# Optimization experiments

Hardware: AMD Instinct MI355X
Metric: run time of the kernel (lower is better)

The kernel has to match this reference:

```python
import jax, jax.numpy as jnp
import numpy as np

GROUP_SIZE = 128


def _unpack_int4(packed):
    # packed: [..., P] int32, each holding 8 int4 nibbles (LSB-first).
    u = jax.lax.bitcast_convert_type(packed, jnp.uint32)
    shifts = jnp.arange(8, dtype=jnp.uint32) * 4  # nibble bit offsets
    vals = (u[..., None] >> shifts) & jnp.uint32(15)  # [..., P, 8]
    return vals.reshape(*packed.shape[:-1], -1)  # [..., P*8] in [0, 15]


def setup_inputs() -> dict:
    key = jax.random.key(0)
    k1, k2, k3, k4 = jax.random.split(key, 4)
    B, S, K, O = 4, 16, 4096, 11008
    G = K // GROUP_SIZE          # 32 groups
    GP = (G + 7) // 8            # 4 packed-zero columns
    imax = np.iinfo(np.int32).max
    x = jax.random.normal(k1, (B, S, K), dtype=jnp.float16)
    qweight_i32 = jax.random.randint(k2, (O, K // 8), 0, imax, dtype=jnp.int32)
    qzeros_i32 = jax.random.randint(k3, (O, GP), 0, imax, dtype=jnp.int32)
    scales_f16 = jax.random.uniform(k4, (O, G), dtype=jnp.float16,
                                    minval=0.001, maxval=0.02)
    return {"x": x, "qweight_i32": qweight_i32, "qzeros_i32": qzeros_i32,
            "scales_f16": scales_f16}


def reference(x, qweight_i32, qzeros_i32, scales_f16):
    O, G = scales_f16.shape
    K = G * GROUP_SIZE
    # Dequantize: w = (q - z) * s, per-group int4 quantization.
    q = _unpack_int4(qweight_i32)[:, :K].astype(jnp.float16)       # [O, K]
    z = _unpack_int4(qzeros_i32)[:, :G].astype(jnp.float16)        # [O, G]
    z_k = jnp.repeat(z, GROUP_SIZE, axis=1)                        # [O, K]
    s_k = jnp.repeat(scales_f16, GROUP_SIZE, axis=1)               # [O, K]
    w = (q - z_k) * s_k                                            # fp16 [O, K]
    x2d = x.reshape(-1, K).astype(jnp.float16)                     # [m, K]
    out = jnp.matmul(x2d, w.T).astype(jnp.float32)                 # [m, O]
    return out.reshape(*x.shape[:-1], O)
```

## Files before the change

kernel.cpp:

```cpp
#include <hip/hip_runtime.h>
#include <stdint.h>

typedef _Float16 half8  __attribute__((ext_vector_type(8)));
typedef _Float16 half2v __attribute__((ext_vector_type(2)));
typedef float    floatx4 __attribute__((ext_vector_type(4)));
typedef uint32_t uint4v  __attribute__((ext_vector_type(4)));

#define KDIM   4096
#define ODIM   11008
#define NG     32
#define K8     512
#define KU     (KDIM/8)
#define KSPLIT 8
#define GPB    4
#define OBLK   172

__global__ void zero_out_kernel(float4* __restrict__ out) {
    out[(size_t)blockIdx.x * 256 + threadIdx.x] = float4{0.f, 0.f, 0.f, 0.f};
}

__device__ __forceinline__ uint32_t pk_f16(float a, float b) {
    return __builtin_bit_cast(uint32_t, __builtin_amdgcn_cvt_pkrtz(a, b));
}

__global__ __launch_bounds__(256) void cvt_x_kernel(
    const float4* __restrict__ x, uint4v* __restrict__ xh)
{
    const size_t i = (size_t)blockIdx.x * 256 + threadIdx.x;
    const float4 f0 = x[2 * i];
    const float4 f1 = x[2 * i + 1];
    xh[i] = uint4v{pk_f16(f0.x, f0.y), pk_f16(f0.z, f0.w),
                   pk_f16(f1.x, f1.y), pk_f16(f1.z, f1.w)};
}

struct GBuf { uint4v a[4]; uint4v u[4]; };

__global__ __launch_bounds__(256, 4) void w4a16_kernel(
    const uint4v*   __restrict__ xh,
    const uint32_t* __restrict__ qw,
    const uint32_t* __restrict__ qz,
    const float*    __restrict__ sc,
    float*          __restrict__ out)
{
    const int t    = threadIdx.x;
    const int wv   = t >> 6;
    const int lane = t & 63;
    const int q    = lane >> 4;
    const int ml   = lane & 15;

    const int ob = blockIdx.x % OBLK;
    const int kb = blockIdx.x / OBLK;
    const int o0 = ob * 64;
    const int g0 = kb * GPB;
    const int m  = wv * 16 + ml;

    const uint4v*   xp  = xh + (size_t)m * KU + (size_t)g0 * 16 + q * 4;
    const uint32_t* qwp = qw + (size_t)(o0 + ml) * K8 + (size_t)g0 * 16 + q * 4;

    uint32_t zdw[4];
    floatx4  svec[4];
    #pragma unroll
    for (int sub = 0; sub < 4; ++sub) {
        const int o = o0 + sub * 16 + ml;
        zdw[sub]  = qz[(size_t)o * 4 + (g0 >> 3)];
        svec[sub] = *reinterpret_cast<const floatx4*>(sc + (size_t)o * NG + g0);
    }
    const int zsh0 = (kb & 1) * 16;

    floatx4 acc[4] = {{0.f,0.f,0.f,0.f},{0.f,0.f,0.f,0.f},
                      {0.f,0.f,0.f,0.f},{0.f,0.f,0.f,0.f}};

    GBuf buf[2];

    auto load_g = [&](int g, GBuf& B) {
        #pragma unroll
        for (int ks = 0; ks < 4; ++ks)
            B.a[ks] = xp[g * 16 + ks];
        #pragma unroll
        for (int sub = 0; sub < 4; ++sub)
            B.u[sub] = *reinterpret_cast<const uint4v*>(
                qwp + (size_t)sub * 16 * K8 + g * 16);
    };

    load_g(0, buf[0]);

    #pragma unroll
    for (int g = 0; g < GPB; ++g) {
        if (g + 1 < GPB) load_g(g + 1, buf[(g + 1) & 1]);
        GBuf& B = buf[g & 1];

        half8 afrag[4];
        #pragma unroll
        for (int ks = 0; ks < 4; ++ks)
            afrag[ks] = __builtin_bit_cast(half8, B.a[ks]);

        #pragma unroll
        for (int sub = 0; sub < 4; ++sub) {
            const uint32_t zh = 0x6400u | ((zdw[sub] >> (zsh0 + g * 4)) & 0xFu);
            const half2v   cz = __builtin_bit_cast(half2v, zh | (zh << 16));
            const float    s  = svec[sub][g];

            floatx4 tmp = {0.f, 0.f, 0.f, 0.f};
            #pragma unroll
            for (int ks = 0; ks < 4; ++ks) {
                const uint32_t ud = B.u[sub][ks];
                const uint32_t t0 = ( ud        & 0x000F000Fu) | 0x64006400u;
                const uint32_t t1 = ((ud >> 4)  & 0x000F000Fu) | 0x64006400u;
                const uint32_t t2 = ((ud >> 8)  & 0x000F000Fu) | 0x64006400u;
                const uint32_t t3 = ((ud >> 12) & 0x000F000Fu) | 0x64006400u;
                const uint32_t p0 = __builtin_amdgcn_perm(t1, t0, 0x05040100u);
                const uint32_t p1 = __builtin_amdgcn_perm(t3, t2, 0x05040100u);
                const uint32_t p2 = __builtin_amdgcn_perm(t1, t0, 0x07060302u);
                const uint32_t p3 = __builtin_amdgcn_perm(t3, t2, 0x07060302u);
                const half2v w0 = __builtin_bit_cast(half2v, p0) - cz;
                const half2v w1 = __builtin_bit_cast(half2v, p1) - cz;
                const half2v w2 = __builtin_bit_cast(half2v, p2) - cz;
                const half2v w3 = __builtin_bit_cast(half2v, p3) - cz;
                const uint4v bw = {__builtin_bit_cast(uint32_t, w0),
                                   __builtin_bit_cast(uint32_t, w1),
                                   __builtin_bit_cast(uint32_t, w2),
                                   __builtin_bit_cast(uint32_t, w3)};
                const half8 b = __builtin_bit_cast(half8, bw);
                tmp = __builtin_amdgcn_mfma_f32_16x16x32_f16(afrag[ks], b, tmp, 0, 0, 0);
            }
            acc[sub][0] += s * tmp[0];
            acc[sub][1] += s * tmp[1];
            acc[sub][2] += s * tmp[2];
            acc[sub][3] += s * tmp[3];
        }
    }

    const int mrow = wv * 16 + q * 4;
    #pragma unroll
    for (int sub = 0; sub < 4; ++sub) {
        float* op = out + (size_t)mrow * ODIM + (o0 + sub * 16 + ml);
        atomicAdd(op,                  acc[sub][0]);
        atomicAdd(op + (size_t)ODIM,   acc[sub][1]);
        atomicAdd(op + 2*(size_t)ODIM, acc[sub][2]);
        atomicAdd(op + 3*(size_t)ODIM, acc[sub][3]);
    }
}

extern "C" void kernel_launch(void* const* d_in, const int* in_sizes, int n_in,
                              void* d_out, int out_size, void* d_ws, size_t ws_size,
                              hipStream_t stream) {
    const float*    x       = (const float*)d_in[0];
    const uint32_t* qweight = (const uint32_t*)d_in[1];
    const uint32_t* qzeros  = (const uint32_t*)d_in[2];
    const float*    scales  = (const float*)d_in[3];
    float* out = (float*)d_out;
    uint4v* xh = (uint4v*)d_ws;

    cvt_x_kernel<<<dim3(128), dim3(256), 0, stream>>>((const float4*)x, xh);
    zero_out_kernel<<<dim3(688), dim3(256), 0, stream>>>((float4*)out);
    w4a16_kernel<<<dim3(OBLK * KSPLIT), dim3(256), 0, stream>>>(
        xh, qweight, qzeros, scales, out);
}
```

Baseline: 110.1 us.

## Fold zero-point subtraction into precomputed activation group sums

The int4 dequant now feeds the raw 1024+q fp16 values straight into the MFMA. The 1024+zero offset is removed afterwards using per-group activation sums that the conversion kernel computes and stores transposed. The x fp16 layout is interleaved so each nibble lines up with its activation without perm instructions. The K split doubles, with fewer groups per block. This trades the per-element subtract and permute work for an extra sum buffer, more atomics, and possible precision loss from the large 1024 offset in fp16/fp32 cancellation.

Result: slower. 122.7 us (+11.5%).

```diff
diff --git a/kernel.cpp b/kernel.cpp
--- a/kernel.cpp
+++ b/kernel.cpp
@@ -2,7 +2,7 @@
 #include <stdint.h>
 
 typedef _Float16 half8  __attribute__((ext_vector_type(8)));
-typedef _Float16 half2v __attribute__((ext_vector_type(2)));
+typedef float    floatx2 __attribute__((ext_vector_type(2)));
 typedef float    floatx4 __attribute__((ext_vector_type(4)));
 typedef uint32_t uint4v  __attribute__((ext_vector_type(4)));
 
@@ -10,9 +10,9 @@
 #define ODIM   11008
 #define NG     32
 #define K8     512
-#define KU     (KDIM/8)
-#define KSPLIT 8
-#define GPB    4
+#define KU     512
+#define KSPLIT 16
+#define GPB    2
 #define OBLK   172
 
 __global__ void zero_out_kernel(float4* __restrict__ out) {
@@ -24,13 +24,26 @@
 }
 
 __global__ __launch_bounds__(256) void cvt_x_kernel(
-    const float4* __restrict__ x, uint4v* __restrict__ xh)
+    const float4* __restrict__ x, uint4v* __restrict__ xh,
+    float* __restrict__ xsumT)
 {
     const size_t i = (size_t)blockIdx.x * 256 + threadIdx.x;
     const float4 f0 = x[2 * i];
     const float4 f1 = x[2 * i + 1];
-    xh[i] = uint4v{pk_f16(f0.x, f0.y), pk_f16(f0.z, f0.w),
-                   pk_f16(f1.x, f1.y), pk_f16(f1.z, f1.w)};
+    xh[i] = uint4v{pk_f16(f0.x, f1.x), pk_f16(f0.y, f1.y),
+                   pk_f16(f0.z, f1.z), pk_f16(f0.w, f1.w)};
+
+    float p = f0.x + f0.y + f0.z + f0.w + f1.x + f1.y + f1.z + f1.w;
+    p += __shfl_xor(p, 1);
+    p += __shfl_xor(p, 2);
+    p += __shfl_xor(p, 4);
+    p += __shfl_xor(p, 8);
+    if ((threadIdx.x & 15) == 0) {
+        const size_t k0 = i * 8;
+        const int m = (int)(k0 >> 12);
+        const int g = (int)(k0 >> 7) & 31;
+        xsumT[g * 64 + m] = p;
+    }
 }
 
 struct GBuf { uint4v a[4]; uint4v u[4]; };
@@ -40,6 +53,7 @@
     const uint32_t* __restrict__ qw,
     const uint32_t* __restrict__ qz,
     const float*    __restrict__ sc,
+    const float*    __restrict__ xsumT,
     float*          __restrict__ out)
 {
     const int t    = threadIdx.x;
@@ -58,20 +72,25 @@
     const uint32_t* qwp = qw + (size_t)(o0 + ml) * K8 + (size_t)g0 * 16 + q * 4;
 
     uint32_t zdw[4];
-    floatx4  svec[4];
+    floatx2  svec[4];
     #pragma unroll
     for (int sub = 0; sub < 4; ++sub) {
         const int o = o0 + sub * 16 + ml;
         zdw[sub]  = qz[(size_t)o * 4 + (g0 >> 3)];
-        svec[sub] = *reinterpret_cast<const floatx4*>(sc + (size_t)o * NG + g0);
+        svec[sub] = *reinterpret_cast<const floatx2*>(sc + (size_t)o * NG + g0);
     }
-    const int zsh0 = (kb & 1) * 16;
+    const int zsh0 = (g0 & 7) * 4;
+
+    const int mrow = wv * 16 + q * 4;
+    floatx4 xsv[GPB];
+    #pragma unroll
+    for (int g = 0; g < GPB; ++g)
+        xsv[g] = *reinterpret_cast<const floatx4*>(xsumT + (g0 + g) * 64 + mrow);
 
     floatx4 acc[4] = {{0.f,0.f,0.f,0.f},{0.f,0.f,0.f,0.f},
                       {0.f,0.f,0.f,0.f},{0.f,0.f,0.f,0.f}};
 
     GBuf buf[2];
-
     auto load_g = [&](int g, GBuf& B) {
         #pragma unroll
         for (int ks = 0; ks < 4; ++ks)
@@ -96,41 +115,30 @@
 
         #pragma unroll
         for (int sub = 0; sub < 4; ++sub) {
-            const uint32_t zh = 0x6400u | ((zdw[sub] >> (zsh0 + g * 4)) & 0xFu);
-            const half2v   cz = __builtin_bit_cast(half2v, zh | (zh << 16));
+            const uint32_t zn = (zdw[sub] >> (zsh0 + g * 4)) & 0xFu;
             const float    s  = svec[sub][g];
+            const float    czs = s * (1024.0f + (float)zn);
 
             floatx4 tmp = {0.f, 0.f, 0.f, 0.f};
             #pragma unroll
             for (int ks = 0; ks < 4; ++ks) {
                 const uint32_t ud = B.u[sub][ks];
-                const uint32_t t0 = ( ud        & 0x000F000Fu) | 0x64006400u;
-                const uint32_t t1 = ((ud >> 4)  & 0x000F000Fu) | 0x64006400u;
-                const uint32_t t2 = ((ud >> 8)  & 0x000F000Fu) | 0x64006400u;
-                const uint32_t t3 = ((ud >> 12) & 0x000F000Fu) | 0x64006400u;
-                const uint32_t p0 = __builtin_amdgcn_perm(t1, t0, 0x05040100u);
-                const uint32_t p1 = __builtin_amdgcn_perm(t3, t2, 0x05040100u);
-                const uint32_t p2 = __builtin_amdgcn_perm(t1, t0, 0x07060302u);
-                const uint32_t p3 = __builtin_amdgcn_perm(t3, t2, 0x07060302u);
-                const half2v w0 = __builtin_bit_cast(half2v, p0) - cz;
-                const half2v w1 = __builtin_bit_cast(half2v, p1) - cz;
-                const half2v w2 = __builtin_bit_cast(half2v, p2) - cz;
-                const half2v w3 = __builtin_bit_cast(half2v, p3) - cz;
-                const uint4v bw = {__builtin_bit_cast(uint32_t, w0),
-                                   __builtin_bit_cast(uint32_t, w1),
-                                   __builtin_bit_cast(uint32_t, w2),
-                                   __builtin_bit_cast(uint32_t, w3)};
+                const uint4v bw = {
+                    ( ud         & 0x000F000Fu) | 0x64006400u,
+                    ((ud >> 4)   & 0x000F000Fu) | 0x64006400u,
+                    ((ud >> 8)   & 0x000F000Fu) | 0x64006400u,
+                    ((ud >> 12)  & 0x000F000Fu) | 0x64006400u};
                 const half8 b = __builtin_bit_cast(half8, bw);
                 tmp = __builtin_amdgcn_mfma_f32_16x16x32_f16(afrag[ks], b, tmp, 0, 0, 0);
             }
-            acc[sub][0] += s * tmp[0];
-            acc[sub][1] += s * tmp[1];
-            acc[sub][2] += s * tmp[2];
-            acc[sub][3] += s * tmp[3];
+            #pragma unroll
+            for (int r = 0; r < 4; ++r) {
+                acc[sub][r] += s * tmp[r];
+                acc[sub][r] -= czs * xsv[g][r];
+            }
         }
     }
 
-    const int mrow = wv * 16 + q * 4;
     #pragma unroll
     for (int sub = 0; sub < 4; ++sub) {
         float* op = out + (size_t)mrow * ODIM + (o0 + sub * 16 + ml);
@@ -149,10 +157,11 @@
     const uint32_t* qzeros  = (const uint32_t*)d_in[2];
     const float*    scales  = (const float*)d_in[3];
     float* out = (float*)d_out;
-    uint4v* xh = (uint4v*)d_ws;
+    uint4v* xh    = (uint4v*)d_ws;
+    float*  xsumT = (float*)((char*)d_ws + 512 * 1024);
 
-    cvt_x_kernel<<<dim3(128), dim3(256), 0, stream>>>((const float4*)x, xh);
+    cvt_x_kernel<<<dim3(128), dim3(256), 0, stream>>>((const float4*)x, xh, xsumT);
     zero_out_kernel<<<dim3(688), dim3(256), 0, stream>>>((float4*)out);
     w4a16_kernel<<<dim3(OBLK * KSPLIT), dim3(256), 0, stream>>>(
-        xh, qweight, qzeros, scales, out);
+        xh, qweight, qzeros, scales, xsumT, out);
 }
```
